# Performance work log

Hardware: AMD Instinct MI355X
Metric: run time of the kernel (lower is better)

## Reference

```python
import jax, jax.numpy as jnp
import numpy as np

NEG_BIG = -9e15
LRELU_SLOPE = 0.2  # alpha

N = 8192
IN_F = 256
OUT_F = 128


def setup_inputs() -> dict:
    key = jax.random.key(0)
    k1, k2, k3, k4 = jax.random.split(key, 4)
    inputs = jax.random.normal(k1, (N, IN_F), dtype=jnp.float32)
    adj = jax.random.randint(k2, (N, N), 0, 2, dtype=jnp.int32)
    # xavier_uniform with gain=1.414
    gain = 1.414
    bW = gain * np.sqrt(6.0 / (IN_F + OUT_F))
    W = jax.random.uniform(k3, (IN_F, OUT_F), minval=-bW, maxval=bW, dtype=jnp.float32)
    ba = gain * np.sqrt(6.0 / (2 * OUT_F + 1))
    a = jax.random.uniform(k4, (2 * OUT_F, 1), minval=-ba, maxval=ba, dtype=jnp.float32)
    return {"inputs": inputs, "adj": adj, "W": W, "a": a}


def reference(inputs, adj, W, a):
    # h: [N, F']
    h = inputs @ W
    # a^T [h_i || h_j] = h_i . a[:F'] + h_j . a[F':]  -- avoids the O(N^2 * 2F') concat
    a1 = a[:OUT_F, 0]   # [F']
    a2 = a[OUT_F:, 0]   # [F']
    s1 = h @ a1         # [N]
    s2 = h @ a2         # [N]
    e = s1[:, None] + s2[None, :]                      # [N, N]
    e = jnp.where(e >= 0, e, LRELU_SLOPE * e)          # LeakyReLU(alpha)
    scores = jnp.where(adj > 0, e, jnp.float32(NEG_BIG))
    attention = jax.nn.softmax(scores, axis=1)         # row softmax; dropout p=0
    h_prime = attention @ h                            # [N, F']
    return jax.nn.elu(h_prime)                         # concat=True -> elu
```

## Files before the change

kernel.cpp:

```cpp
#include <hip/hip_runtime.h>
#include <hip/hip_bf16.h>

#define NN   8192
#define INF_ 256
#define OUTF 128
#define SLOPE 0.2f
#define NC   4
#define CHJ  2048
#define NP   16

typedef float f32x4  __attribute__((ext_vector_type(4)));
typedef float f32x16 __attribute__((ext_vector_type(16)));
typedef short bf16x8 __attribute__((ext_vector_type(8)));
typedef int   i32x4  __attribute__((ext_vector_type(4)));
typedef unsigned int u32;
typedef unsigned short u16;
typedef u16 u16x2 __attribute__((ext_vector_type(2)));

__device__ __forceinline__ u16 f2bf(float f) {
  return __builtin_bit_cast(u16, __float2bfloat16(f));
}


__global__ __launch_bounds__(256) void gat_k1(
    const float* __restrict__ X, const float* __restrict__ W,
    const float* __restrict__ a, u16* __restrict__ hbF,
    float* __restrict__ s1, float* __restrict__ s2) {
  __shared__ float xs[16 * INF_];
  const int t = threadIdx.x;
  const int r0 = blockIdx.x * 16;
  {
    const f32x4* src = (const f32x4*)(X + (size_t)r0 * INF_);
    f32x4* dst = (f32x4*)xs;
#pragma unroll
    for (int i = 0; i < 4; i++) dst[t + 256 * i] = src[t + 256 * i];
  }
  __syncthreads();
  const int cg = t & 31;
  const int rg = t >> 5;
  float acc[2][4];
#pragma unroll
  for (int i = 0; i < 2; i++)
#pragma unroll
    for (int j = 0; j < 4; j++) acc[i][j] = 0.f;

  for (int k = 0; k < INF_; k += 4) {
    f32x4 xv[2];
#pragma unroll
    for (int i = 0; i < 2; i++) xv[i] = *(const f32x4*)&xs[(rg * 2 + i) * INF_ + k];
#pragma unroll
    for (int kk = 0; kk < 4; kk++) {
      f32x4 wv = *(const f32x4*)&W[(k + kk) * OUTF + cg * 4];
#pragma unroll
      for (int i = 0; i < 2; i++)
#pragma unroll
        for (int j = 0; j < 4; j++) acc[i][j] = fmaf(xv[i][kk], wv[j], acc[i][j]);
    }
  }

  f32x4 a1v = *(const f32x4*)&a[cg * 4];
  f32x4 a2v = *(const f32x4*)&a[OUTF + cg * 4];
  float p1[2], p2[2];
#pragma unroll
  for (int i = 0; i < 2; i++) {
    p1[i] = acc[i][0] * a1v[0] + acc[i][1] * a1v[1] + acc[i][2] * a1v[2] + acc[i][3] * a1v[3];
    p2[i] = acc[i][0] * a2v[0] + acc[i][1] * a2v[1] + acc[i][2] * a2v[2] + acc[i][3] * a2v[3];
  }
#pragma unroll
  for (int m = 1; m < 32; m <<= 1) {
#pragma unroll
    for (int i = 0; i < 2; i++) {
      p1[i] += __shfl_xor(p1[i], m);
      p2[i] += __shfl_xor(p2[i], m);
    }
  }
  if (cg == 0) {
#pragma unroll
    for (int i = 0; i < 2; i++) {
      s1[r0 + rg * 2 + i] = p1[i];
      s2[r0 + rg * 2 + i] = p2[i];
    }
  }

  const int R0 = r0 + rg * 2;
  const int c  = R0 >> 11;
  const int pr = (R0 >> 7) & 15;
  const int tt = (R0 >> 3) & 15;
  const int e0 = R0 & 7;
  const int n  = (c * 8 + (pr >> 1)) * 16 + tt;
  const int lg = (pr & 1) * 32;
#pragma unroll
  for (int j = 0; j < 4; j++) {
    const int C = cg * 4 + j;
    u16x2 pk = {f2bf(acc[0][j]), f2bf(acc[1][j])};
    *(u16x2*)(hbF + ((size_t)(n * 4 + (C >> 5)) * 64 + lg + (C & 31)) * 8 + e0) = pk;
  }
}

__global__ __launch_bounds__(256) void gat_k2(const float* __restrict__ s2,
                                              float* __restrict__ bmax,
                                              float* __restrict__ E1,
                                              float* __restrict__ E2) {
  __shared__ float sm[4];
  const int t = threadIdx.x;
  const int i = blockIdx.x * 256 + t;
  f32x4 v = ((const f32x4*)s2)[i];
  f32x4 e1, e2;
  float m = -1e30f;
#pragma unroll
  for (int k = 0; k < 4; k++) {
    m = fmaxf(m, v[k]);
    e1[k] = __expf(v[k]);
    e2[k] = __expf(SLOPE * v[k]);
  }
  ((f32x4*)E1)[i] = e1;
  ((f32x4*)E2)[i] = e2;
#pragma unroll
  for (int k = 1; k < 64; k <<= 1) m = fmaxf(m, __shfl_xor(m, k));
  if ((t & 63) == 0) sm[t >> 6] = m;
  __syncthreads();
  if (t == 0)
    bmax[blockIdx.x] = fmaxf(fmaxf(sm[0], sm[1]), fmaxf(sm[2], sm[3]));
}

__device__ __forceinline__ void st16(float* dst, const f32x16& A, int g) {
#pragma unroll
  for (int r = 0; r < 16; r++) {
    const int dr = (r & 3) + 8 * (r >> 2) + 4 * g;
    dst[dr * 128] = A[r];
  }
}
__device__ __forceinline__ void ad16(float* dst, const f32x16& A, int g) {
#pragma unroll
  for (int r = 0; r < 16; r++) {
    const int dr = (r & 3) + 8 * (r >> 2) + 4 * g;
    dst[dr * 128] += A[r];
  }
}

__global__ __launch_bounds__(512, 2) void gat_k3(
    const int* __restrict__ adj, const u16* __restrict__ hbF,
    const float* __restrict__ s1g, const float* __restrict__ E1,
    const float* __restrict__ E2, const float* __restrict__ bmax,
    float* __restrict__ out) {
  __shared__ unsigned char mb[2][8192];
  __shared__ float lred[8192];
  __shared__ float dred[288];
  const int t = threadIdx.x;
  const int w = t >> 6;
  const int l = t & 63;
  const int r0 = blockIdx.x * 32;
  const int row = l & 31;
  const int g = l >> 5;
  const int pr = 2 * w + g;

  float s2m = bmax[0];
#pragma unroll
  for (int k = 1; k < 8; k++) s2m = fmaxf(s2m, bmax[k]);
  const float s1r = s1g[r0 + row];
  float Mi = s1r + s2m;
  Mi = fmaxf(Mi, SLOPE * Mi);
  const float A = __expf(s1r - Mi);
  const float B = __expf(SLOPE * s1r - Mi);

  const int srow = t >> 4;
  const int cl = t & 15;
  const int* gsrc = adj + (size_t)(r0 + srow) * NN + cl * 8;
  const int wslot = ((0) ^ (srow & 15));

  i32x4 sA0, sA1, sB0, sB1;
#define LOADP(S0, S1, C, P)                                  \
  {                                                          \
    const int* p_ = gsrc + (C) * CHJ + (P) * 128;            \
    S0 = *(const i32x4*)(p_);                                \
    S1 = *(const i32x4*)(p_ + 4);                            \
  }
#define PACKP(S0, S1, P, NB)                                               \
  {                                                                        \
    unsigned b_ = 0;                                                       \
    _Pragma("unroll") for (int e_ = 0; e_ < 4; e_++) {                     \
      b_ |= (S0[e_] > 0 ? 1u : 0u) << e_;                                  \
      b_ |= (S1[e_] > 0 ? 1u : 0u) << (e_ + 4);                            \
    }                                                                      \
    mb[NB][srow * 256 + (((P) ^ (srow & 15)) << 4) + cl] = (unsigned char)b_; \
  }

  f32x16 acc0 = 0.f, acc1 = 0.f, acc2 = 0.f, acc3 = 0.f;
  float dsA = 0.f, dsB = 0.f;

#define COMPUTE(CC, TT, BMV)                                                 \
  {                                                                          \
    const unsigned b = ((unsigned)(BMV)[(TT) >> 2] >> (((TT)&3) * 8)) & 0xffu; \
    const u16* bqb = hbF + (size_t)(((CC)*8 + w) * 16 + (TT)) * 2048 + l * 8; \
    bf16x8 b0 = *(const bf16x8*)(bqb);                                       \
    bf16x8 b1 = *(const bf16x8*)(bqb + 512);                                 \
    bf16x8 b2 = *(const bf16x8*)(bqb + 1024);                                \
    bf16x8 b3 = *(const bf16x8*)(bqb + 1536);                                \
    const float* e1q = E1 + (CC)*CHJ + pr * 128 + (TT)*8;                    \
    const float* e2q = E2 + (CC)*CHJ + pr * 128 + (TT)*8;                    \
    f32x4 u0 = *(const f32x4*)(e1q);                                         \
    f32x4 u1 = *(const f32x4*)(e1q + 4);                                     \
    f32x4 v0 = *(const f32x4*)(e2q);                                         \
    f32x4 v1 = *(const f32x4*)(e2q + 4);                                     \
    const float uu[8] = {u0[0], u0[1], u0[2], u0[3], u1[0], u1[1], u1[2], u1[3]}; \
    const float vv[8] = {v0[0], v0[1], v0[2], v0[3], v1[0], v1[1], v1[2], v1[3]}; \
    u32 aw[4];                                                               \
    _Pragma("unroll") for (int e = 0; e < 8; e += 2) {                       \
      float pa = fmaxf(A * uu[e], B * vv[e]);                                \
      float pb = fmaxf(A * uu[e + 1], B * vv[e + 1]);                        \
      pa = (b & (1u << e)) ? pa : 0.f;                                       \
      pb = (b & (1u << (e + 1))) ? pb : 0.f;                                 \
      dsA += pa;                                                             \
      dsB += pb;                                                             \
      aw[e >> 1] = __builtin_amdgcn_perm(                                    \
          __builtin_bit_cast(u32, pb) + 0x8000u,                             \
          __builtin_bit_cast(u32, pa) + 0x8000u, 0x07060302u);               \
    }                                                                        \
    const bf16x8 af = __builtin_bit_cast(                                    \
        bf16x8, (i32x4){(int)aw[0], (int)aw[1], (int)aw[2], (int)aw[3]});    \
    acc0 = __builtin_amdgcn_mfma_f32_32x32x16_bf16(af, b0, acc0, 0, 0, 0);   \
    acc1 = __builtin_amdgcn_mfma_f32_32x32x16_bf16(af, b1, acc1, 0, 0, 0);   \
    acc2 = __builtin_amdgcn_mfma_f32_32x32x16_bf16(af, b2, acc2, 0, 0, 0);   \
    acc3 = __builtin_amdgcn_mfma_f32_32x32x16_bf16(af, b3, acc3, 0, 0, 0);   \
  }

  LOADP(sA0, sA1, 0, 0);
  LOADP(sB0, sB1, 0, 1);
#pragma unroll
  for (int p = 2; p < NP; p += 2) {
    PACKP(sA0, sA1, p - 2, 0);
    LOADP(sA0, sA1, 0, p);
    PACKP(sB0, sB1, p - 1, 0);
    LOADP(sB0, sB1, 0, p + 1);
  }
  PACKP(sA0, sA1, 14, 0);
  PACKP(sB0, sB1, 15, 0);
  __syncthreads();

  for (int c = 0; c < NC; c++) {
    const int cb = c & 1, nb = cb ^ 1;
    const i32x4 bmv =
        *(const i32x4*)&mb[cb][row * 256 + ((pr ^ (row & 15)) << 4)];
    const bool more = (c + 1 < NC);

#pragma unroll
    for (int th = 0; th < 8; th++) {
      const int t0 = th * 2, t1 = t0 + 1;
      if (more) {
        if (t0 >= 2) PACKP(sA0, sA1, t0 - 2, nb);
        LOADP(sA0, sA1, c + 1, t0);
      }
      COMPUTE(c, t0, bmv);
      if (more) {
        if (t1 >= 2) PACKP(sB0, sB1, t1 - 2, nb);
        LOADP(sB0, sB1, c + 1, t1);
      }
      COMPUTE(c, t1, bmv);
    }
    if (more) {
      PACKP(sA0, sA1, 14, nb);
      PACKP(sB0, sB1, 15, nb);
    }
    __syncthreads();
  }

  float dsum = dsA + dsB;
  dsum += __shfl_xor(dsum, 32);
  if (l < 32) dred[w * 32 + l] = dsum;

  const int colw = l & 31;
  if (w < 2) {
    st16(&lred[w * 4096 + 0 * 32 + colw], acc0, g);
    st16(&lred[w * 4096 + 1 * 32 + colw], acc1, g);
    st16(&lred[w * 4096 + 2 * 32 + colw], acc2, g);
    st16(&lred[w * 4096 + 3 * 32 + colw], acc3, g);
  }
  __syncthreads();
  if (t < 32) {
    float d = 0.f;
#pragma unroll
    for (int w8 = 0; w8 < 8; w8++) d += dred[w8 * 32 + t];
    dred[256 + t] = d;
  }
  if (w == 2 || w == 3) {
    ad16(&lred[(w - 2) * 4096 + 0 * 32 + colw], acc0, g);
    ad16(&lred[(w - 2) * 4096 + 1 * 32 + colw], acc1, g);
    ad16(&lred[(w - 2) * 4096 + 2 * 32 + colw], acc2, g);
    ad16(&lred[(w - 2) * 4096 + 3 * 32 + colw], acc3, g);
  }
  __syncthreads();
  if (w == 4 || w == 5) {
    ad16(&lred[(w - 4) * 4096 + 0 * 32 + colw], acc0, g);
    ad16(&lred[(w - 4) * 4096 + 1 * 32 + colw], acc1, g);
    ad16(&lred[(w - 4) * 4096 + 2 * 32 + colw], acc2, g);
    ad16(&lred[(w - 4) * 4096 + 3 * 32 + colw], acc3, g);
  }
  __syncthreads();
  if (w == 6 || w == 7) {
    ad16(&lred[(w - 6) * 4096 + 0 * 32 + colw], acc0, g);
    ad16(&lred[(w - 6) * 4096 + 1 * 32 + colw], acc1, g);
    ad16(&lred[(w - 6) * 4096 + 2 * 32 + colw], acc2, g);
    ad16(&lred[(w - 6) * 4096 + 3 * 32 + colw], acc3, g);
  }
  __syncthreads();

  const float myden = fmaxf(dred[256 + (t >> 4)], 1e-30f);
  const int flat = t * 8;
  float o[8];
#pragma unroll
  for (int i = 0; i < 4; i++) {
    o[i] = lred[flat + i] + lred[4096 + flat + i];
    o[4 + i] = lred[flat + 4 + i] + lred[4096 + flat + 4 + i];
  }
  f32x4 ra, rb;
#pragma unroll
  for (int i = 0; i < 4; i++) {
    float va = o[i] / myden;
    float vb = o[4 + i] / myden;
    ra[i] = (va > 0.f) ? va : expm1f(va);
    rb[i] = (vb > 0.f) ? vb : expm1f(vb);
  }
  float* op = out + (size_t)(r0 + (t >> 4)) * OUTF + (t & 15) * 8;
  *(f32x4*)op = ra;
  *(f32x4*)(op + 4) = rb;
}

extern "C" void kernel_launch(void* const* d_in, const int* in_sizes, int n_in,
                              void* d_out, int out_size, void* d_ws, size_t ws_size,
                              hipStream_t stream) {
  (void)in_sizes; (void)n_in; (void)out_size; (void)ws_size;
  const float* X  = (const float*)d_in[0];
  const int*  adj = (const int*)d_in[1];
  const float* W  = (const float*)d_in[2];
  const float* a  = (const float*)d_in[3];
  float* out = (float*)d_out;

  char* ws = (char*)d_ws;
  u16*   hbF  = (u16*)ws;
  float* s1   = (float*)(ws + (2u << 20));
  float* s2   = (float*)(ws + (2u << 20) + (32u << 10));
  float* bmax = (float*)(ws + (2u << 20) + (64u << 10));
  float* E1   = (float*)(ws + (2u << 20) + (128u << 10));
  float* E2   = (float*)(ws + (2u << 20) + (160u << 10));

  gat_k1<<<NN / 16, 256, 0, stream>>>(X, W, a, hbF, s1, s2);
  gat_k2<<<8, 256, 0, stream>>>(s2, bmax, E1, E2);
  gat_k3<<<NN / 32, 512, 0, stream>>>(adj, hbF, s1, E1, E2, bmax, out);
}
```

Baseline: 116.2 us.

## Split attention columns across two blocks per row tile with partial-sum reduction kernel

The main attention kernel now splits the neighbor dimension in half, launching two blocks per 32-row tile, each handling two 2048-column chunks. Each block writes partial numerators and denominators to workspace, and a new kernel combines them, normalizes and applies ELU. Launch bounds are raised to allow 4 blocks per CU. The goal is more parallelism, since only 256 blocks ran before on a many-CU GPU. In exchange it adds an extra kernel launch and an 8 MB partial-buffer write and read.

```diff
diff --git a/kernel.cpp b/kernel.cpp
--- a/kernel.cpp
+++ b/kernel.cpp
@@ -5,7 +5,7 @@
 #define INF_ 256
 #define OUTF 128
 #define SLOPE 0.2f
-#define NC   4
+#define NCH  2
 #define CHJ  2048
 #define NP   16
 
@@ -83,11 +83,11 @@
   }
 
   const int R0 = r0 + rg * 2;
-  const int c  = R0 >> 11;
+  const int cc = R0 >> 11;
   const int pr = (R0 >> 7) & 15;
   const int tt = (R0 >> 3) & 15;
   const int e0 = R0 & 7;
-  const int n  = (c * 8 + (pr >> 1)) * 16 + tt;
+  const int n  = (cc * 8 + (pr >> 1)) * 16 + tt;
   const int lg = (pr & 1) * 32;
 #pragma unroll
   for (int j = 0; j < 4; j++) {
@@ -138,18 +138,20 @@
   }
 }
 
-__global__ __launch_bounds__(512, 2) void gat_k3(
+__global__ __launch_bounds__(512, 4) void gat_k3(
     const int* __restrict__ adj, const u16* __restrict__ hbF,
     const float* __restrict__ s1g, const float* __restrict__ E1,
     const float* __restrict__ E2, const float* __restrict__ bmax,
-    float* __restrict__ out) {
+    float* __restrict__ part, float* __restrict__ dpart) {
   __shared__ unsigned char mb[2][8192];
   __shared__ float lred[8192];
-  __shared__ float dred[288];
+  __shared__ float dred[256];
   const int t = threadIdx.x;
   const int w = t >> 6;
   const int l = t & 63;
-  const int r0 = blockIdx.x * 32;
+  const int rb = blockIdx.x >> 1;
+  const int jh = blockIdx.x & 1;
+  const int r0 = rb * 32;
   const int row = l & 31;
   const int g = l >> 5;
   const int pr = 2 * w + g;
@@ -165,8 +167,7 @@
 
   const int srow = t >> 4;
   const int cl = t & 15;
-  const int* gsrc = adj + (size_t)(r0 + srow) * NN + cl * 8;
-  const int wslot = ((0) ^ (srow & 15));
+  const int* gsrc = adj + (size_t)(r0 + srow) * NN + jh * (NCH * CHJ) + cl * 8;
 
   i32x4 sA0, sA1, sB0, sB1;
 #define LOADP(S0, S1, C, P)                                  \
@@ -175,53 +176,55 @@
     S0 = *(const i32x4*)(p_);                                \
     S1 = *(const i32x4*)(p_ + 4);                            \
   }
-#define PACKP(S0, S1, P, NB)                                               \
-  {                                                                        \
-    unsigned b_ = 0;                                                       \
-    _Pragma("unroll") for (int e_ = 0; e_ < 4; e_++) {                     \
-      b_ |= (S0[e_] > 0 ? 1u : 0u) << e_;                                  \
-      b_ |= (S1[e_] > 0 ? 1u : 0u) << (e_ + 4);                            \
-    }                                                                      \
+#define PACKP(S0, S1, P, NB)                                                  \
+  {                                                                           \
+    unsigned b_ = 0;                                                          \
+    _Pragma("unroll") for (int e_ = 0; e_ < 4; e_++) {                        \
+      b_ |= (S0[e_] > 0 ? 1u : 0u) << e_;                                     \
+      b_ |= (S1[e_] > 0 ? 1u : 0u) << (e_ + 4);                               \
+    }                                                                         \
     mb[NB][srow * 256 + (((P) ^ (srow & 15)) << 4) + cl] = (unsigned char)b_; \
   }
 
   f32x16 acc0 = 0.f, acc1 = 0.f, acc2 = 0.f, acc3 = 0.f;
-  float dsA = 0.f, dsB = 0.f;
-
-#define COMPUTE(CC, TT, BMV)                                                 \
-  {                                                                          \
+  float dsum = 0.f;
+
+#define COMPUTE(CC, TT, BMV)                                                   \
+  {                                                                            \
     const unsigned b = ((unsigned)(BMV)[(TT) >> 2] >> (((TT)&3) * 8)) & 0xffu; \
-    const u16* bqb = hbF + (size_t)(((CC)*8 + w) * 16 + (TT)) * 2048 + l * 8; \
-    bf16x8 b0 = *(const bf16x8*)(bqb);                                       \
-    bf16x8 b1 = *(const bf16x8*)(bqb + 512);                                 \
-    bf16x8 b2 = *(const bf16x8*)(bqb + 1024);                                \
-    bf16x8 b3 = *(const bf16x8*)(bqb + 1536);                                \
-    const float* e1q = E1 + (CC)*CHJ + pr * 128 + (TT)*8;                    \
-    const float* e2q = E2 + (CC)*CHJ + pr * 128 + (TT)*8;                    \
-    f32x4 u0 = *(const f32x4*)(e1q);                                         \
-    f32x4 u1 = *(const f32x4*)(e1q + 4);                                     \
-    f32x4 v0 = *(const f32x4*)(e2q);                                         \
-    f32x4 v1 = *(const f32x4*)(e2q + 4);                                     \
-    const float uu[8] = {u0[0], u0[1], u0[2], u0[3], u1[0], u1[1], u1[2], u1[3]}; \
-    const float vv[8] = {v0[0], v0[1], v0[2], v0[3], v1[0], v1[1], v1[2], v1[3]}; \
-    u32 aw[4];                                                               \
-    _Pragma("unroll") for (int e = 0; e < 8; e += 2) {                       \
-      float pa = fmaxf(A * uu[e], B * vv[e]);                                \
-      float pb = fmaxf(A * uu[e + 1], B * vv[e + 1]);                        \
-      pa = (b & (1u << e)) ? pa : 0.f;                                       \
-      pb = (b & (1u << (e + 1))) ? pb : 0.f;                                 \
-      dsA += pa;                                                             \
-      dsB += pb;                                                             \
-      aw[e >> 1] = __builtin_amdgcn_perm(                                    \
-          __builtin_bit_cast(u32, pb) + 0x8000u,                             \
-          __builtin_bit_cast(u32, pa) + 0x8000u, 0x07060302u);               \
-    }                                                                        \
-    const bf16x8 af = __builtin_bit_cast(                                    \
-        bf16x8, (i32x4){(int)aw[0], (int)aw[1], (int)aw[2], (int)aw[3]});    \
-    acc0 = __builtin_amdgcn_mfma_f32_32x32x16_bf16(af, b0, acc0, 0, 0, 0);   \
-    acc1 = __builtin_amdgcn_mfma_f32_32x32x16_bf16(af, b1, acc1, 0, 0, 0);   \
-    acc2 = __builtin_amdgcn_mfma_f32_32x32x16_bf16(af, b2, acc2, 0, 0, 0);   \
-    acc3 = __builtin_amdgcn_mfma_f32_32x32x16_bf16(af, b3, acc3, 0, 0, 0);   \
+    const u16* bqb = hbF + (size_t)(((CC)*8 + w) * 16 + (TT)) * 2048 + l * 8;  \
+    bf16x8 b0 = *(const bf16x8*)(bqb);                                         \
+    bf16x8 b1 = *(const bf16x8*)(bqb + 512);                                   \
+    bf16x8 b2 = *(const bf16x8*)(bqb + 1024);                                  \
+    bf16x8 b3 = *(const bf16x8*)(bqb + 1536);                                  \
+    const float* e1q = E1 + (CC)*CHJ + pr * 128 + (TT)*8;                      \
+    const float* e2q = E2 + (CC)*CHJ + pr * 128 + (TT)*8;                      \
+    f32x4 u0 = *(const f32x4*)(e1q);                                           \
+    f32x4 u1 = *(const f32x4*)(e1q + 4);                                       \
+    f32x4 v0 = *(const f32x4*)(e2q);                                           \
+    f32x4 v1 = *(const f32x4*)(e2q + 4);                                       \
+    u32 aw[4];                                                                 \
+    _Pragma("unroll") for (int e = 0; e < 8; e += 2) {                         \
+      const float ue0 = (e < 4) ? u0[e & 3] : u1[e & 3];                       \
+      const float ue1 = (e < 4) ? u0[(e + 1) & 3] : u1[(e + 1) & 3];           \
+      const float ve0 = (e < 4) ? v0[e & 3] : v1[e & 3];                       \
+      const float ve1 = (e < 4) ? v0[(e + 1) & 3] : v1[(e + 1) & 3];           \
+      float pa = fmaxf(A * ue0, B * ve0);                                      \
+      float pb = fmaxf(A * ue1, B * ve1);                                      \
+      pa = (b & (1u << e)) ? pa : 0.f;                                         \
+      pb = (b & (1u << (e + 1))) ? pb : 0.f;                                   \
+      dsum += pa;                                                              \
+      dsum += pb;                                                              \
+      aw[e >> 1] = __builtin_amdgcn_perm(                                      \
+          __builtin_bit_cast(u32, pb) + 0x8000u,                               \
+          __builtin_bit_cast(u32, pa) + 0x8000u, 0x07060302u);                 \
+    }                                                                          \
+    const bf16x8 af = __builtin_bit_cast(                                      \
+        bf16x8, (i32x4){(int)aw[0], (int)aw[1], (int)aw[2], (int)aw[3]});      \
+    acc0 = __builtin_amdgcn_mfma_f32_32x32x16_bf16(af, b0, acc0, 0, 0, 0);     \
+    acc1 = __builtin_amdgcn_mfma_f32_32x32x16_bf16(af, b1, acc1, 0, 0, 0);     \
+    acc2 = __builtin_amdgcn_mfma_f32_32x32x16_bf16(af, b2, acc2, 0, 0, 0);     \
+    acc3 = __builtin_amdgcn_mfma_f32_32x32x16_bf16(af, b3, acc3, 0, 0, 0);     \
   }
 
   LOADP(sA0, sA1, 0, 0);
@@ -237,34 +240,34 @@
   PACKP(sB0, sB1, 15, 0);
   __syncthreads();
 
-  for (int c = 0; c < NC; c++) {
-    const int cb = c & 1, nb = cb ^ 1;
+  const int cc0 = jh * NCH;
+  const int cc1 = cc0 + 1;
+
+  {
     const i32x4 bmv =
-        *(const i32x4*)&mb[cb][row * 256 + ((pr ^ (row & 15)) << 4)];
-    const bool more = (c + 1 < NC);
-
+        *(const i32x4*)&mb[0][row * 256 + ((pr ^ (row & 15)) << 4)];
 #pragma unroll
     for (int th = 0; th < 8; th++) {
       const int t0 = th * 2, t1 = t0 + 1;
-      if (more) {
-        if (t0 >= 2) PACKP(sA0, sA1, t0 - 2, nb);
-        LOADP(sA0, sA1, c + 1, t0);
-      }
-      COMPUTE(c, t0, bmv);
-      if (more) {
-        if (t1 >= 2) PACKP(sB0, sB1, t1 - 2, nb);
-        LOADP(sB0, sB1, c + 1, t1);
-      }
-      COMPUTE(c, t1, bmv);
+      if (t0 >= 2) PACKP(sA0, sA1, t0 - 2, 1);
+      LOADP(sA0, sA1, 1, t0);
+      COMPUTE(cc0, t0, bmv);
+      if (t1 >= 2) PACKP(sB0, sB1, t1 - 2, 1);
+      LOADP(sB0, sB1, 1, t1);
+      COMPUTE(cc0, t1, bmv);
     }
-    if (more) {
-      PACKP(sA0, sA1, 14, nb);
-      PACKP(sB0, sB1, 15, nb);
-    }
+    PACKP(sA0, sA1, 14, 1);
+    PACKP(sB0, sB1, 15, 1);
     __syncthreads();
   }
 
-  float dsum = dsA + dsB;
+  {
+    const i32x4 bmv =
+        *(const i32x4*)&mb[1][row * 256 + ((pr ^ (row & 15)) << 4)];
+#pragma unroll
+    for (int tt = 0; tt < NP; tt++) COMPUTE(cc1, tt, bmv);
+  }
+
   dsum += __shfl_xor(dsum, 32);
   if (l < 32) dred[w * 32 + l] = dsum;
 
@@ -280,7 +283,7 @@
     float d = 0.f;
 #pragma unroll
     for (int w8 = 0; w8 < 8; w8++) d += dred[w8 * 32 + t];
-    dred[256 + t] = d;
+    dpart[jh * NN + r0 + t] = d;
   }
   if (w == 2 || w == 3) {
     ad16(&lred[(w - 2) * 4096 + 0 * 32 + colw], acc0, g);
@@ -304,25 +307,33 @@
   }
   __syncthreads();
 
-  const float myden = fmaxf(dred[256 + (t >> 4)], 1e-30f);
   const int flat = t * 8;
-  float o[8];
-#pragma unroll
-  for (int i = 0; i < 4; i++) {
-    o[i] = lred[flat + i] + lred[4096 + flat + i];
-    o[4 + i] = lred[flat + 4 + i] + lred[4096 + flat + 4 + i];
-  }
-  f32x4 ra, rb;
-#pragma unroll
-  for (int i = 0; i < 4; i++) {
-    float va = o[i] / myden;
-    float vb = o[4 + i] / myden;
-    ra[i] = (va > 0.f) ? va : expm1f(va);
-    rb[i] = (vb > 0.f) ? vb : expm1f(vb);
-  }
-  float* op = out + (size_t)(r0 + (t >> 4)) * OUTF + (t & 15) * 8;
-  *(f32x4*)op = ra;
-  *(f32x4*)(op + 4) = rb;
+  f32x4 pa = *(f32x4*)&lred[flat];
+  f32x4 pb = *(f32x4*)&lred[flat + 4];
+  pa += *(f32x4*)&lred[4096 + flat];
+  pb += *(f32x4*)&lred[4096 + flat + 4];
+  float* pp = part + (size_t)jh * (NN * OUTF) + (size_t)r0 * OUTF + flat;
+  *(f32x4*)pp = pa;
+  *(f32x4*)(pp + 4) = pb;
+}
+
+__global__ __launch_bounds__(256) void gat_k4(
+    const float* __restrict__ part, const float* __restrict__ dpart,
+    float* __restrict__ out) {
+  const int idx = blockIdx.x * 256 + threadIdx.x;
+  const int e4 = idx * 4;
+  const int i = e4 >> 7;
+  f32x4 p = *(const f32x4*)&part[e4];
+  p += *(const f32x4*)&part[(size_t)(NN * OUTF) + e4];
+  float d = dpart[i] + dpart[NN + i];
+  d = fmaxf(d, 1e-30f);
+  f32x4 r;
+#pragma unroll
+  for (int k = 0; k < 4; k++) {
+    float v = p[k] / d;
+    r[k] = (v > 0.f) ? v : expm1f(v);
+  }
+  *(f32x4*)&out[e4] = r;
 }
 
 extern "C" void kernel_launch(void* const* d_in, const int* in_sizes, int n_in,
@@ -336,14 +347,17 @@
   float* out = (float*)d_out;
 
   char* ws = (char*)d_ws;
-  u16*   hbF  = (u16*)ws;
-  float* s1   = (float*)(ws + (2u << 20));
-  float* s2   = (float*)(ws + (2u << 20) + (32u << 10));
-  float* bmax = (float*)(ws + (2u << 20) + (64u << 10));
-  float* E1   = (float*)(ws + (2u << 20) + (128u << 10));
-  float* E2   = (float*)(ws + (2u << 20) + (160u << 10));
+  u16*   hbF   = (u16*)ws;
+  float* s1    = (float*)(ws + (2u << 20));
+  float* s2    = (float*)(ws + (2u << 20) + (32u << 10));
+  float* bmax  = (float*)(ws + (2u << 20) + (64u << 10));
+  float* E1    = (float*)(ws + (2u << 20) + (128u << 10));
+  float* E2    = (float*)(ws + (2u << 20) + (160u << 10));
+  float* dpart = (float*)(ws + (2u << 20) + (192u << 10));
+  float* part  = (float*)(ws + (4u << 20));
 
   gat_k1<<<NN / 16, 256, 0, stream>>>(X, W, a, hbF, s1, s2);
   gat_k2<<<8, 256, 0, stream>>>(s2, bmax, E1, E2);
-  gat_k3<<<NN / 32, 512, 0, stream>>>(adj, hbF, s1, E1, E2, bmax, out);
-}
+  gat_k3<<<512, 512, 0, stream>>>(adj, hbF, s1, E1, E2, bmax, part, dpart);
+  gat_k4<<<(NN * OUTF / 4) / 256, 256, 0, stream>>>(part, dpart, out);
+}
```

After: 330.9 us. 2.85x slower.
